# Optimization experiments

Measured on AMD Instinct MI355X. Metric: run time of the kernel, lower is better.

## Reference

```python
import jax, jax.numpy as jnp
import numpy as np

EPS = 1e-5  # torch GroupNorm default eps


def _pairwise_sqdist(x, y):
    # squared euclidean distance matrix, clamped at 0 for numerical safety
    d = (jnp.sum(x * x, -1)[:, None] + jnp.sum(y * y, -1)[None, :]
         - 2.0 * (x @ y.T))
    return jnp.maximum(d, 0.0)


def _pc_normalize(ref, src):
    # jointly center and scale both clouds to the unit sphere
    pts = jnp.concatenate([ref, src], axis=0)
    centroid = pts.mean(axis=0, keepdims=True)
    pts = pts - centroid
    m = jnp.max(jnp.linalg.norm(pts, axis=1))
    pts = pts / m
    n_ref = ref.shape[0]
    return pts[:n_ref], pts[n_ref:]


def _group_norm(x, gamma, beta, groups):
    N, C = x.shape
    xg = x.reshape(N, groups, C // groups)
    mean = xg.mean(-1, keepdims=True)
    var = jnp.mean((xg - mean) ** 2, -1, keepdims=True)
    xn = ((xg - mean) / jnp.sqrt(var + EPS)).reshape(N, C)
    return xn * gamma + beta


def setup_inputs() -> dict:
    key = jax.random.key(0)
    ks = jax.random.split(key, 8)
    N_ref, N_src, D = 128, 128, 256
    points_c = jax.random.normal(ks[0], (N_ref + N_src, 3), jnp.float32)
    ref_feats = jax.random.normal(ks[1], (N_ref, D), jnp.float32)
    src_feats = jax.random.normal(ks[2], (N_src, D), jnp.float32)
    # normalized features, as the '_norm' names suggest
    ref_feats = ref_feats / jnp.linalg.norm(ref_feats, axis=-1, keepdims=True)
    src_feats = src_feats / jnp.linalg.norm(src_feats, axis=-1, keepdims=True)
    # a valid rigid transform: random rotation + small translation
    A = jax.random.normal(ks[3], (3, 3), jnp.float32)
    Q, _ = jnp.linalg.qr(A)
    trans = jnp.eye(4, dtype=jnp.float32)
    trans = trans.at[:3, :3].set(Q)
    trans = trans.at[:3, 3].set(jax.random.normal(ks[4], (3,), jnp.float32) * 0.1)
    s = 1.0 / np.sqrt(512)
    return {
        'points_c': points_c,
        'ref_feats_c_norm': ref_feats,
        'src_feats_c_norm': src_feats,
        'trans': trans,
        'W1': jax.random.normal(ks[5], (256, 512), jnp.float32) * s,
        'b1': jnp.zeros((256,), jnp.float32),
        'g1': jnp.ones((256,), jnp.float32),
        'bt1': jnp.zeros((256,), jnp.float32),
        'W2': jax.random.normal(ks[6], (128, 256), jnp.float32) * (1.0 / np.sqrt(256)),
        'b2': jnp.zeros((128,), jnp.float32),
        'g2': jnp.ones((128,), jnp.float32),
        'bt2': jnp.zeros((128,), jnp.float32),
        'W3': jax.random.normal(ks[7], (2, 128), jnp.float32) * (1.0 / np.sqrt(128)),
        'b3': jnp.zeros((2,), jnp.float32),
        'ref_length': 128,
    }


def reference(points_c, ref_feats_c_norm, src_feats_c_norm, trans,
              W1, b1, g1, bt1, W2, b2, g2, bt2, W3, b3, ref_length):
    GROUPS = 8
    ref_points = points_c[:ref_length]
    src_points = points_c[ref_length:]
    # apply rigid transform to src points
    src_points = src_points @ trans[:3, :3].T + trans[:3, 3]
    ref_n, src_n = _pc_normalize(ref_points, src_points)

    dist_mat = jnp.exp(-_pairwise_sqdist(ref_n, src_n))  # [Nr, Ns]
    match_idx_ref = jnp.argmax(dist_mat, axis=1)
    match_idx_src = jnp.argmax(dist_mat, axis=0)
    min_dist_ref = jnp.max(dist_mat, axis=1)
    min_dist_src = jnp.max(dist_mat, axis=0)

    feat_score_mat = ref_feats_c_norm @ src_feats_c_norm.T  # [Nr, Ns]
    feat_match_idx_ref = jnp.argmax(feat_score_mat, axis=1)
    feat_match_idx_src = jnp.argmax(feat_score_mat, axis=0)
    feat_match_ref = jnp.max(feat_score_mat, axis=1)
    feat_match_src = jnp.max(feat_score_mat, axis=0)

    r_idx = jnp.arange(feat_score_mat.shape[0])
    c_idx = jnp.arange(feat_score_mat.shape[1])
    feat_score_ref = feat_score_mat[r_idx, match_idx_ref]
    feat_score_src = feat_score_mat[match_idx_src, c_idx]
    dist_ref = dist_mat[r_idx, feat_match_idx_ref]
    dist_src = dist_mat[feat_match_idx_src, c_idx]

    min_dist = jnp.concatenate([min_dist_ref, min_dist_src])
    feat_score = jnp.concatenate([feat_score_ref, feat_score_src])
    perm_d = jnp.argsort(-min_dist)  # descending sort
    d_m = min_dist[perm_d] * feat_score[perm_d]

    match_feat = jnp.concatenate([feat_match_ref, feat_match_src])
    match_dist = jnp.concatenate([dist_ref, dist_src])
    perm_f = jnp.argsort(-match_feat)
    m_d = match_dist[perm_f] * match_feat[perm_f]

    geo_out = jnp.concatenate([d_m, m_d])[None, :]  # [1, 512]

    h = _group_norm(geo_out @ W1.T + b1, g1, bt1, GROUPS)
    h = jax.nn.relu(h)
    h = _group_norm(h @ W2.T + b2, g2, bt2, GROUPS)
    h = jax.nn.relu(h)
    return h @ W3.T + b3  # [1, num_classes]
```

## Files before the change

kernel.cpp:

```cpp
#include <hip/hip_runtime.h>
#include <math.h>

#define NREF 128
#define NSRC 128
#define DIM  256
#define EPS  1e-5f

__global__ __launch_bounds__(256) void feat_kernel(
    const float* __restrict__ ref_feats,
    const float* __restrict__ src_feats,
    float* __restrict__ feat_mat)
{
    __shared__ __align__(16) float refrow[DIM];
    const int i = blockIdx.x;
    const int t = threadIdx.x;
    if (t < 64) ((float4*)refrow)[t] = ((const float4*)(ref_feats + i * DIM))[t];
    __syncthreads();

    const int w = t >> 6, l = t & 63;
    const float4 r = ((const float4*)refrow)[l];

    for (int m = 0; m < 32; ++m) {
        const int j = w * 32 + m;
        const float4 a = ((const float4*)(src_feats + j * DIM))[l];
        float acc = a.x * r.x + a.y * r.y + a.z * r.z + a.w * r.w;
        acc += __shfl_down(acc, 32);
        acc += __shfl_down(acc, 16);
        acc += __shfl_down(acc, 8);
        acc += __shfl_down(acc, 4);
        acc += __shfl_down(acc, 2);
        acc += __shfl_down(acc, 1);
        if (l == 0) feat_mat[i * NSRC + j] = acc;
    }
}

__global__ __launch_bounds__(1024) void rest_kernel(
    const float* __restrict__ points_c,
    const float* __restrict__ trans,
    const float* __restrict__ feat_mat,
    const float* __restrict__ W1, const float* __restrict__ b1,
    const float* __restrict__ g1, const float* __restrict__ bt1,
    const float* __restrict__ W2, const float* __restrict__ b2,
    const float* __restrict__ g2, const float* __restrict__ bt2,
    const float* __restrict__ W3, const float* __restrict__ b3,
    float* __restrict__ out)
{
    __shared__ float px[256], py[256], pz[256], nsq[256];
    __shared__ float wred[16];
    __shared__ float red[4];
    __shared__ float pvD[1024]; __shared__ int piD[1024];
    __shared__ float pvF[1024]; __shared__ int piF[1024];
    __shared__ float min_dist[256];   __shared__ int match_idx[256];
    __shared__ float match_feat[256]; __shared__ int feat_idx[256];
    __shared__ float feat_score[256], match_dist[256];
    __shared__ int prD[1024]; __shared__ int prF[1024];
    __shared__ __align__(16) float geo[512];
    __shared__ float y1[256];
    __shared__ __align__(16) float h1[256];
    __shared__ float y2[128], h2[128];

    const int t    = threadIdx.x;
    const int wave = t >> 6;
    const int lane = t & 63;

    float x = 0.f, y = 0.f, z = 0.f;
    if (t < 256) {
        x = points_c[3 * t + 0];
        y = points_c[3 * t + 1];
        z = points_c[3 * t + 2];
        if (t >= NREF) {
            float nx = trans[0] * x + trans[1] * y + trans[2]  * z + trans[3];
            float ny = trans[4] * x + trans[5] * y + trans[6]  * z + trans[7];
            float nz = trans[8] * x + trans[9] * y + trans[10] * z + trans[11];
            x = nx; y = ny; z = nz;
        }
        float sx = x, sy = y, sz = z;
        for (int off = 32; off >= 1; off >>= 1) {
            sx += __shfl_down(sx, off);
            sy += __shfl_down(sy, off);
            sz += __shfl_down(sz, off);
        }
        if (lane == 0) {
            wred[wave]     = sx;
            wred[4 + wave] = sy;
            wred[8 + wave] = sz;
        }
    }
    __syncthreads();
    if (t == 0) {
        red[0] = (wred[0] + wred[1] + wred[2] + wred[3]) * (1.0f / 256.0f);
        red[1] = (wred[4] + wred[5] + wred[6] + wred[7]) * (1.0f / 256.0f);
        red[2] = (wred[8] + wred[9] + wred[10] + wred[11]) * (1.0f / 256.0f);
    }
    __syncthreads();

    if (t < 256) {
        x -= red[0]; y -= red[1]; z -= red[2];
        float n = x * x + y * y + z * z;
        float mx = n;
        for (int off = 32; off >= 1; off >>= 1)
            mx = fmaxf(mx, __shfl_down(mx, off));
        if (lane == 0) wred[wave] = mx;
    }
    __syncthreads();
    if (t == 0)
        red[3] = 1.0f / sqrtf(fmaxf(fmaxf(wred[0], wred[1]), fmaxf(wred[2], wred[3])));
    __syncthreads();
    if (t < 256) {
        const float inv = red[3];
        x *= inv; y *= inv; z *= inv;
        px[t] = x; py[t] = y; pz[t] = z;
        nsq[t] = x * x + y * y + z * z;
    }
    __syncthreads();

    {
        const int rc = t & 255, q = t >> 8;
        float bdv = -1.f; int bdi = 0;
        float bfv = -2.f; int bfi = 0;
        if (rc < 128) {
            const int i = rc;
            for (int m = 0; m < 32; ++m) {
                const int j = q * 32 + m;
                float d = nsq[i] + nsq[128 + j]
                        - 2.0f * (px[i] * px[128 + j] + py[i] * py[128 + j] + pz[i] * pz[128 + j]);
                d = fmaxf(d, 0.f);
                const float v = expf(-d);
                if (v > bdv) { bdv = v; bdi = j; }
                const float f = feat_mat[i * NSRC + j];
                if (f > bfv) { bfv = f; bfi = j; }
            }
        } else {
            const int j = rc - 128;
            for (int m = 0; m < 32; ++m) {
                const int i = q * 32 + m;
                float d = nsq[i] + nsq[128 + j]
                        - 2.0f * (px[i] * px[128 + j] + py[i] * py[128 + j] + pz[i] * pz[128 + j]);
                d = fmaxf(d, 0.f);
                const float v = expf(-d);
                if (v > bdv) { bdv = v; bdi = i; }
                const float f = feat_mat[i * NSRC + j];
                if (f > bfv) { bfv = f; bfi = i; }
            }
        }
        pvD[q * 256 + rc] = bdv; piD[q * 256 + rc] = bdi;
        pvF[q * 256 + rc] = bfv; piF[q * 256 + rc] = bfi;
    }
    __syncthreads();

    if (t < 256) {
        float bv = -1.f; int bi = 0;
        for (int q = 0; q < 4; ++q) {
            const float v = pvD[q * 256 + t];
            if (v > bv) { bv = v; bi = piD[q * 256 + t]; }
        }
        min_dist[t] = bv; match_idx[t] = bi;
        float fv = -2.f; int fi = 0;
        for (int q = 0; q < 4; ++q) {
            const float v = pvF[q * 256 + t];
            if (v > fv) { fv = v; fi = piF[q * 256 + t]; }
        }
        match_feat[t] = fv; feat_idx[t] = fi;
    }
    __syncthreads();

    if (t < 256) {
        if (t < NREF) {
            const int i = t;
            feat_score[t] = feat_mat[i * NSRC + match_idx[t]];
            const int j = feat_idx[t];
            float d = nsq[i] + nsq[128 + j]
                    - 2.0f * (px[i] * px[128 + j] + py[i] * py[128 + j] + pz[i] * pz[128 + j]);
            d = fmaxf(d, 0.f);
            match_dist[t] = expf(-d);
        } else {
            const int j = t - 128;
            feat_score[t] = feat_mat[match_idx[t] * NSRC + j];
            const int i = feat_idx[t];
            float d = nsq[i] + nsq[128 + j]
                    - 2.0f * (px[i] * px[128 + j] + py[i] * py[128 + j] + pz[i] * pz[128 + j]);
            d = fmaxf(d, 0.f);
            match_dist[t] = expf(-d);
        }
    }
    __syncthreads();

    {
        const int e = t & 255, q = t >> 8;
        const float v  = min_dist[e];
        const float wv = match_feat[e];
        int r1 = 0, r2 = 0;
        for (int m = 0; m < 64; ++m) {
            const int j = q * 64 + m;
            const float u  = min_dist[j];
            r1 += (u > v) || (u == v && j < e);
            const float uf = match_feat[j];
            r2 += (uf > wv) || (uf == wv && j < e);
        }
        prD[q * 256 + e] = r1;
        prF[q * 256 + e] = r2;
    }
    __syncthreads();
    if (t < 256) {
        const int r  = prD[t] + prD[256 + t] + prD[512 + t] + prD[768 + t];
        geo[r] = min_dist[t] * feat_score[t];
        const int rf = prF[t] + prF[256 + t] + prF[512 + t] + prF[768 + t];
        geo[256 + rf] = match_dist[t] * match_feat[t];
    }
    __syncthreads();

    {
        const float4* __restrict__ geo4 = (const float4*)geo;
        const float4 ga = geo4[lane];
        const float4 gb = geo4[64 + lane];
        for (int cc = 0; cc < 16; ++cc) {
            const int c = (wave << 4) + cc;
            const float4* __restrict__ wrow = (const float4*)(W1 + c * 512);
            const float4 a = wrow[lane];
            const float4 b = wrow[64 + lane];
            float acc = a.x * ga.x + a.y * ga.y + a.z * ga.z + a.w * ga.w
                      + b.x * gb.x + b.y * gb.y + b.z * gb.z + b.w * gb.w;
            acc += __shfl_down(acc, 32);
            acc += __shfl_down(acc, 16);
            acc += __shfl_down(acc, 8);
            acc += __shfl_down(acc, 4);
            acc += __shfl_down(acc, 2);
            acc += __shfl_down(acc, 1);
            if (lane == 0) y1[c] = acc + b1[c];
        }
    }
    __syncthreads();
    if (t < 256) {
        const int g = t >> 5;
        float s = 0.f;
        for (int k = 0; k < 32; ++k) s += y1[(g << 5) + k];
        const float mean = s * (1.0f / 32.0f);
        float q = 0.f;
        for (int k = 0; k < 32; ++k) { const float d = y1[(g << 5) + k] - mean; q += d * d; }
        const float var = q * (1.0f / 32.0f);
        const float xn = (y1[t] - mean) * rsqrtf(var + EPS);
        h1[t] = fmaxf(xn * g1[t] + bt1[t], 0.f);
    }
    __syncthreads();

    {
        const float4* __restrict__ h1v = (const float4*)h1;
        const float4 ha = h1v[lane];
        for (int cc = 0; cc < 8; ++cc) {
            const int c = (wave << 3) + cc;
            const float4 a = ((const float4*)(W2 + c * 256))[lane];
            float acc = a.x * ha.x + a.y * ha.y + a.z * ha.z + a.w * ha.w;
            acc += __shfl_down(acc, 32);
            acc += __shfl_down(acc, 16);
            acc += __shfl_down(acc, 8);
            acc += __shfl_down(acc, 4);
            acc += __shfl_down(acc, 2);
            acc += __shfl_down(acc, 1);
            if (lane == 0) y2[c] = acc + b2[c];
        }
    }
    __syncthreads();
    if (t < 128) {
        const int g = t >> 4;
        float s = 0.f;
        for (int k = 0; k < 16; ++k) s += y2[(g << 4) + k];
        const float mean = s * (1.0f / 16.0f);
        float q = 0.f;
        for (int k = 0; k < 16; ++k) { const float d = y2[(g << 4) + k] - mean; q += d * d; }
        const float var = q * (1.0f / 16.0f);
        const float xn = (y2[t] - mean) * rsqrtf(var + EPS);
        h2[t] = fmaxf(xn * g2[t] + bt2[t], 0.f);
    }
    __syncthreads();

    if (wave < 2) {
        float acc = W3[wave * 128 + lane] * h2[lane]
                  + W3[wave * 128 + 64 + lane] * h2[64 + lane];
        acc += __shfl_down(acc, 32);
        acc += __shfl_down(acc, 16);
        acc += __shfl_down(acc, 8);
        acc += __shfl_down(acc, 4);
        acc += __shfl_down(acc, 2);
        acc += __shfl_down(acc, 1);
        if (lane == 0) out[wave] = acc + b3[wave];
    }
}

extern "C" void kernel_launch(void* const* d_in, const int* in_sizes, int n_in,
                              void* d_out, int out_size, void* d_ws, size_t ws_size,
                              hipStream_t stream)
{
    const float* points_c  = (const float*)d_in[0];
    const float* ref_feats = (const float*)d_in[1];
    const float* src_feats = (const float*)d_in[2];
    const float* trans     = (const float*)d_in[3];
    const float* W1  = (const float*)d_in[4];
    const float* b1  = (const float*)d_in[5];
    const float* g1  = (const float*)d_in[6];
    const float* bt1 = (const float*)d_in[7];
    const float* W2  = (const float*)d_in[8];
    const float* b2  = (const float*)d_in[9];
    const float* g2  = (const float*)d_in[10];
    const float* bt2 = (const float*)d_in[11];
    const float* W3  = (const float*)d_in[12];
    const float* b3  = (const float*)d_in[13];

    float* feat_mat = (float*)d_ws;

    feat_kernel<<<dim3(NREF), dim3(256), 0, stream>>>(ref_feats, src_feats, feat_mat);
    rest_kernel<<<dim3(1), dim3(1024), 0, stream>>>(
        points_c, trans, feat_mat,
        W1, b1, g1, bt1, W2, b2, g2, bt2, W3, b3,
        (float*)d_out);
}
```

Measured before the change: 130.2 us.

## Split single-block MLP tail into multi-block kernels and widen feat kernel

```diff
diff --git a/kernel.cpp b/kernel.cpp
--- a/kernel.cpp
+++ b/kernel.cpp
@@ -6,7 +6,7 @@
 #define DIM  256
 #define EPS  1e-5f
 
-__global__ __launch_bounds__(256) void feat_kernel(
+__global__ __launch_bounds__(512) void feat_kernel(
     const float* __restrict__ ref_feats,
     const float* __restrict__ src_feats,
     float* __restrict__ feat_mat)
@@ -20,30 +20,29 @@
     const int w = t >> 6, l = t & 63;
     const float4 r = ((const float4*)refrow)[l];
 
-    for (int m = 0; m < 32; ++m) {
-        const int j = w * 32 + m;
-        const float4 a = ((const float4*)(src_feats + j * DIM))[l];
-        float acc = a.x * r.x + a.y * r.y + a.z * r.z + a.w * r.w;
-        acc += __shfl_down(acc, 32);
-        acc += __shfl_down(acc, 16);
-        acc += __shfl_down(acc, 8);
-        acc += __shfl_down(acc, 4);
-        acc += __shfl_down(acc, 2);
-        acc += __shfl_down(acc, 1);
-        if (l == 0) feat_mat[i * NSRC + j] = acc;
-    }
-}
-
-__global__ __launch_bounds__(1024) void rest_kernel(
+    for (int m = 0; m < 16; m += 2) {
+        const int j0 = w * 16 + m;
+        const int j1 = j0 + 1;
+        const float4 a0 = ((const float4*)(src_feats + j0 * DIM))[l];
+        const float4 a1 = ((const float4*)(src_feats + j1 * DIM))[l];
+        float acc0 = a0.x * r.x + a0.y * r.y + a0.z * r.z + a0.w * r.w;
+        float acc1 = a1.x * r.x + a1.y * r.y + a1.z * r.z + a1.w * r.w;
+        for (int off = 32; off >= 1; off >>= 1) {
+            acc0 += __shfl_down(acc0, off);
+            acc1 += __shfl_down(acc1, off);
+        }
+        if (l == 0) {
+            feat_mat[i * NSRC + j0] = acc0;
+            feat_mat[i * NSRC + j1] = acc1;
+        }
+    }
+}
+
+__global__ __launch_bounds__(1024) void geo_kernel(
     const float* __restrict__ points_c,
     const float* __restrict__ trans,
     const float* __restrict__ feat_mat,
-    const float* __restrict__ W1, const float* __restrict__ b1,
-    const float* __restrict__ g1, const float* __restrict__ bt1,
-    const float* __restrict__ W2, const float* __restrict__ b2,
-    const float* __restrict__ g2, const float* __restrict__ bt2,
-    const float* __restrict__ W3, const float* __restrict__ b3,
-    float* __restrict__ out)
+    float* __restrict__ geo_out)
 {
     __shared__ float px[256], py[256], pz[256], nsq[256];
     __shared__ float wred[16];
@@ -54,10 +53,6 @@
     __shared__ float match_feat[256]; __shared__ int feat_idx[256];
     __shared__ float feat_score[256], match_dist[256];
     __shared__ int prD[1024]; __shared__ int prF[1024];
-    __shared__ __align__(16) float geo[512];
-    __shared__ float y1[256];
-    __shared__ __align__(16) float h1[256];
-    __shared__ float y2[128], h2[128];
 
     const int t    = threadIdx.x;
     const int wave = t >> 6;
@@ -203,87 +198,109 @@
     __syncthreads();
     if (t < 256) {
         const int r  = prD[t] + prD[256 + t] + prD[512 + t] + prD[768 + t];
-        geo[r] = min_dist[t] * feat_score[t];
+        geo_out[r] = min_dist[t] * feat_score[t];
         const int rf = prF[t] + prF[256 + t] + prF[512 + t] + prF[768 + t];
-        geo[256 + rf] = match_dist[t] * match_feat[t];
-    }
-    __syncthreads();
-
-    {
-        const float4* __restrict__ geo4 = (const float4*)geo;
-        const float4 ga = geo4[lane];
-        const float4 gb = geo4[64 + lane];
-        for (int cc = 0; cc < 16; ++cc) {
-            const int c = (wave << 4) + cc;
-            const float4* __restrict__ wrow = (const float4*)(W1 + c * 512);
-            const float4 a = wrow[lane];
-            const float4 b = wrow[64 + lane];
-            float acc = a.x * ga.x + a.y * ga.y + a.z * ga.z + a.w * ga.w
-                      + b.x * gb.x + b.y * gb.y + b.z * gb.z + b.w * gb.w;
-            acc += __shfl_down(acc, 32);
-            acc += __shfl_down(acc, 16);
-            acc += __shfl_down(acc, 8);
-            acc += __shfl_down(acc, 4);
-            acc += __shfl_down(acc, 2);
-            acc += __shfl_down(acc, 1);
-            if (lane == 0) y1[c] = acc + b1[c];
-        }
-    }
-    __syncthreads();
-    if (t < 256) {
-        const int g = t >> 5;
+        geo_out[256 + rf] = match_dist[t] * match_feat[t];
+    }
+}
+
+__global__ __launch_bounds__(64) void mlp1_kernel(
+    const float* __restrict__ geo,
+    const float* __restrict__ W1, const float* __restrict__ b1,
+    float* __restrict__ y1)
+{
+    const int c = blockIdx.x, l = threadIdx.x;
+    const float4 ga = ((const float4*)geo)[l];
+    const float4 gb = ((const float4*)geo)[64 + l];
+    const float4* __restrict__ wrow = (const float4*)(W1 + c * 512);
+    const float4 a = wrow[l];
+    const float4 b = wrow[64 + l];
+    float acc = a.x * ga.x + a.y * ga.y + a.z * ga.z + a.w * ga.w
+              + b.x * gb.x + b.y * gb.y + b.z * gb.z + b.w * gb.w;
+    acc += __shfl_down(acc, 32);
+    acc += __shfl_down(acc, 16);
+    acc += __shfl_down(acc, 8);
+    acc += __shfl_down(acc, 4);
+    acc += __shfl_down(acc, 2);
+    acc += __shfl_down(acc, 1);
+    if (l == 0) y1[c] = acc + b1[c];
+}
+
+__global__ __launch_bounds__(64) void mlp2_kernel(
+    const float* __restrict__ y1,
+    const float* __restrict__ g1, const float* __restrict__ bt1,
+    const float* __restrict__ W2, const float* __restrict__ b2,
+    float* __restrict__ y2)
+{
+    __shared__ __align__(16) float y1s[256];
+    __shared__ float stats[16];
+    const int c = blockIdx.x, l = threadIdx.x;
+    ((float4*)y1s)[l] = ((const float4*)y1)[l];
+    __syncthreads();
+    if (l < 8) {
         float s = 0.f;
-        for (int k = 0; k < 32; ++k) s += y1[(g << 5) + k];
+        for (int k = 0; k < 32; ++k) s += y1s[(l << 5) + k];
         const float mean = s * (1.0f / 32.0f);
         float q = 0.f;
-        for (int k = 0; k < 32; ++k) { const float d = y1[(g << 5) + k] - mean; q += d * d; }
+        for (int k = 0; k < 32; ++k) { const float d = y1s[(l << 5) + k] - mean; q += d * d; }
         const float var = q * (1.0f / 32.0f);
-        const float xn = (y1[t] - mean) * rsqrtf(var + EPS);
-        h1[t] = fmaxf(xn * g1[t] + bt1[t], 0.f);
-    }
-    __syncthreads();
-
+        stats[l] = mean;
+        stats[8 + l] = rsqrtf(var + EPS);
+    }
+    __syncthreads();
+    const float4 gg = ((const float4*)g1)[l];
+    const float4 bb = ((const float4*)bt1)[l];
+    const int g = l >> 3;
+    const float mean = stats[g], inv = stats[8 + g];
+    const float4 yv = ((const float4*)y1s)[l];
+    float4 h;
+    h.x = fmaxf((yv.x - mean) * inv * gg.x + bb.x, 0.f);
+    h.y = fmaxf((yv.y - mean) * inv * gg.y + bb.y, 0.f);
+    h.z = fmaxf((yv.z - mean) * inv * gg.z + bb.z, 0.f);
+    h.w = fmaxf((yv.w - mean) * inv * gg.w + bb.w, 0.f);
+    const float4 wv = ((const float4*)(W2 + c * 256))[l];
+    float acc = wv.x * h.x + wv.y * h.y + wv.z * h.z + wv.w * h.w;
+    acc += __shfl_down(acc, 32);
+    acc += __shfl_down(acc, 16);
+    acc += __shfl_down(acc, 8);
+    acc += __shfl_down(acc, 4);
+    acc += __shfl_down(acc, 2);
+    acc += __shfl_down(acc, 1);
+    if (l == 0) y2[c] = acc + b2[c];
+}
+
+__global__ __launch_bounds__(128) void final_kernel(
+    const float* __restrict__ y2,
+    const float* __restrict__ g2, const float* __restrict__ bt2,
+    const float* __restrict__ W3, const float* __restrict__ b3,
+    float* __restrict__ out)
+{
+    __shared__ float y2s[128], h2[128];
+    const int t = threadIdx.x;
+    y2s[t] = y2[t];
+    __syncthreads();
     {
-        const float4* __restrict__ h1v = (const float4*)h1;
-        const float4 ha = h1v[lane];
-        for (int cc = 0; cc < 8; ++cc) {
-            const int c = (wave << 3) + cc;
-            const float4 a = ((const float4*)(W2 + c * 256))[lane];
-            float acc = a.x * ha.x + a.y * ha.y + a.z * ha.z + a.w * ha.w;
-            acc += __shfl_down(acc, 32);
-            acc += __shfl_down(acc, 16);
-            acc += __shfl_down(acc, 8);
-            acc += __shfl_down(acc, 4);
-            acc += __shfl_down(acc, 2);
-            acc += __shfl_down(acc, 1);
-            if (lane == 0) y2[c] = acc + b2[c];
-        }
-    }
-    __syncthreads();
-    if (t < 128) {
         const int g = t >> 4;
         float s = 0.f;
-        for (int k = 0; k < 16; ++k) s += y2[(g << 4) + k];
+        for (int k = 0; k < 16; ++k) s += y2s[(g << 4) + k];
         const float mean = s * (1.0f / 16.0f);
         float q = 0.f;
-        for (int k = 0; k < 16; ++k) { const float d = y2[(g << 4) + k] - mean; q += d * d; }
+        for (int k = 0; k < 16; ++k) { const float d = y2s[(g << 4) + k] - mean; q += d * d; }
         const float var = q * (1.0f / 16.0f);
-        const float xn = (y2[t] - mean) * rsqrtf(var + EPS);
+        const float xn = (y2s[t] - mean) * rsqrtf(var + EPS);
         h2[t] = fmaxf(xn * g2[t] + bt2[t], 0.f);
     }
     __syncthreads();
-
-    if (wave < 2) {
-        float acc = W3[wave * 128 + lane] * h2[lane]
-                  + W3[wave * 128 + 64 + lane] * h2[64 + lane];
-        acc += __shfl_down(acc, 32);
-        acc += __shfl_down(acc, 16);
-        acc += __shfl_down(acc, 8);
-        acc += __shfl_down(acc, 4);
-        acc += __shfl_down(acc, 2);
-        acc += __shfl_down(acc, 1);
-        if (lane == 0) out[wave] = acc + b3[wave];
-    }
+    const int wave = t >> 6, lane = t & 63;
+    float acc = W3[wave * 128 + lane] * h2[lane]
+              + W3[wave * 128 + 64 + lane] * h2[64 + lane];
+    acc += __shfl_down(acc, 32);
+    acc += __shfl_down(acc, 16);
+    acc += __shfl_down(acc, 8);
+    acc += __shfl_down(acc, 4);
+    acc += __shfl_down(acc, 2);
+    acc += __shfl_down(acc, 1);
+    if (lane == 0) out[wave] = acc + b3[wave];
 }
 
 extern "C" void kernel_launch(void* const* d_in, const int* in_sizes, int n_in,
@@ -306,10 +323,13 @@
     const float* b3  = (const float*)d_in[13];
 
     float* feat_mat = (float*)d_ws;
-
-    feat_kernel<<<dim3(NREF), dim3(256), 0, stream>>>(ref_feats, src_feats, feat_mat);
-    rest_kernel<<<dim3(1), dim3(1024), 0, stream>>>(
-        points_c, trans, feat_mat,
-        W1, b1, g1, bt1, W2, b2, g2, bt2, W3, b3,
-        (float*)d_out);
-}
+    float* geo = feat_mat;
+    float* y1  = feat_mat + 512;
+    float* y2  = feat_mat + 768;
+
+    feat_kernel<<<dim3(NREF), dim3(512), 0, stream>>>(ref_feats, src_feats, feat_mat);
+    geo_kernel<<<dim3(1), dim3(1024), 0, stream>>>(points_c, trans, feat_mat, geo);
+    mlp1_kernel<<<dim3(256), dim3(64), 0, stream>>>(geo, W1, b1, y1);
+    mlp2_kernel<<<dim3(128), dim3(64), 0, stream>>>(y1, g1, bt1, W2, b2, y2);
+    final_kernel<<<dim3(1), dim3(128), 0, stream>>>(y2, g2, bt2, W3, b3, (float*)d_out);
+}
```

Result: faster. 104.5 us (-19.7%).
